# Performance work log

Hardware: AMD Instinct MI355X
Metric: run time of the kernel (lower is better)

Reference implementation:

```python
import jax, jax.numpy as jnp
import numpy as np

B, N, H, NH, P = 32, 400, 512, 8, 3
DK = H // NH
SCALE = DK ** -0.5
EPS = 1e-5


def _ln(x, g, b):
    m = jnp.mean(x, axis=-1, keepdims=True)
    v = jnp.mean((x - m) ** 2, axis=-1, keepdims=True)
    return (x - m) * jax.lax.rsqrt(v + EPS) * g + b


def _split(x):  # [B,N,H] -> [B,h,N,dk]
    return x.reshape(x.shape[0], x.shape[1], NH, DK).transpose(0, 2, 1, 3)


def _merge(x):  # [B,h,N,dk] -> [B,N,H]
    return x.transpose(0, 2, 1, 3).reshape(x.shape[0], x.shape[2], H)


def _attn(q, k, v, mask):
    s = jnp.einsum('bhid,bhjd->bhij', q, k) * SCALE
    s = s * (1.0 + mask[:, None])  # learned multiplicative prior mask
    p = jax.nn.softmax(s, axis=-1)
    return jnp.einsum('bhij,bhjd->bhid', p, v)


def _weight_gen(pri, z, C, wq, keys, wf, bf):
    # pooled token query attends over the num_priors prior matrices
    qv = jnp.mean(z @ wq, axis=1)  # [B,H]
    aw = jax.nn.softmax((qv @ keys.T) * (H ** -0.5), axis=-1)  # [B,P]
    w = jnp.einsum('bp,bpij->bij', aw, pri)  # [B,N,N] fused prior mask
    fused = jnp.einsum('bij,bjh->bih', C, z) @ wf + bf  # [B,N,H] neighborhood fusion
    return w, aw, fused


def _ffn(x, w1, b1, w2, b2):
    return jax.nn.gelu(x @ w1 + b1, approximate=False) @ w2 + b2


def _forward(x_FC, x_SC, pri_FC, pri_SC, FC, SC, dw,
             ln_attn_FC_g, ln_attn_FC_b, ln_attn_SC_g, ln_attn_SC_b,
             ln_ffn_FC_g, ln_ffn_FC_b, ln_ffn_SC_g, ln_ffn_SC_b,
             qkv_FC_w, qkv_SC_w,
             ffn_FC_w1, ffn_FC_b1, ffn_FC_w2, ffn_FC_b2,
             ffn_SC_w1, ffn_SC_b1, ffn_SC_w2, ffn_SC_b2,
             wg_q_w, wg_keys, wg_fuse_w, wg_fuse_b,
             dist_in_FC_w, dist_in_FC_b, dist_in_SC_w, dist_in_SC_b,
             dist_out_FC_w, dist_out_FC_b, dist_out_SC_w, dist_out_SC_b):
    z_FC = _ln(x_FC, ln_attn_FC_g, ln_attn_FC_b)
    z_SC = _ln(x_SC, ln_attn_SC_g, ln_attn_SC_b)
    q_FC, k_FC, v_FC = [_split(t) for t in jnp.split(z_FC @ qkv_FC_w, 3, axis=-1)]
    q_SC, k_SC, v_SC = [_split(t) for t in jnp.split(z_SC @ qkv_SC_w, 3, axis=-1)]
    w_FC, aw_FC, fused_FC = _weight_gen(pri_FC, z_FC, FC, wg_q_w, wg_keys, wg_fuse_w, wg_fuse_b)
    w_SC, aw_SC, fused_SC = _weight_gen(pri_SC, z_SC, SC, wg_q_w, wg_keys, wg_fuse_w, wg_fuse_b)
    ctx_FC = _merge(_attn(q_FC, k_FC, v_FC, w_FC))
    ctx_SC = _merge(_attn(q_SC, k_SC, v_SC, w_SC))
    attn_out_FC = x_FC + ctx_FC + fused_FC
    attn_out_SC = x_SC + ctx_SC + fused_SC
    x_FC_new = attn_out_FC + _ffn(_ln(attn_out_FC, ln_ffn_FC_g, ln_ffn_FC_b), ffn_FC_w1, ffn_FC_b1, ffn_FC_w2, ffn_FC_b2)
    x_SC_new = attn_out_SC + _ffn(_ln(attn_out_SC, ln_ffn_SC_g, ln_ffn_SC_b), ffn_SC_w1, ffn_SC_b1, ffn_SC_w2, ffn_SC_b2)
    wf, ws = dw[0], dw[1]
    proj_FC = x_FC_new @ dist_in_FC_w + dist_in_FC_b
    proj_SC = x_SC_new @ dist_in_SC_w + dist_in_SC_b
    l_FC = jax.nn.log_softmax(proj_FC.reshape(-1, H), axis=-1)
    l_SC = jax.nn.log_softmax(proj_SC.reshape(-1, H), axis=-1)
    p_FC = jnp.exp(l_FC)
    p_SC = jnp.exp(l_SC)
    rows = jnp.float32(l_FC.shape[0])
    kl_FC = jnp.sum(p_SC * (l_SC - l_FC)) / rows  # KLDiv(batchmean)(l_FC, p_SC)
    kl_SC = jnp.sum(p_FC * (l_FC - l_SC)) / rows
    x_FC_out = (1.0 - wf) * x_FC_new + wf * (proj_FC @ dist_out_FC_w + dist_out_FC_b)
    x_SC_out = (1.0 - ws) * x_SC_new + ws * (proj_SC @ dist_out_SC_w + dist_out_SC_b)
    distill_loss = 0.5 * (kl_FC * wf + kl_SC * ws)
    return (x_FC_out, x_SC_out, distill_loss, aw_FC, aw_SC)


def setup_inputs() -> dict:
    key = jax.random.key(0)
    ks = jax.random.split(key, 24)
    init = lambda k, shape: 0.02 * jax.random.normal(k, shape, jnp.float32)
    d = {}
    d['x_FC'] = jax.random.normal(ks[0], (B, N, H), jnp.float32)
    d['x_SC'] = jax.random.normal(ks[1], (B, N, H), jnp.float32)
    d['pri_FC'] = jax.random.uniform(ks[2], (B, P, N, N), jnp.float32)
    d['pri_SC'] = jax.random.uniform(ks[3], (B, P, N, N), jnp.float32)
    d['FC'] = jax.random.uniform(ks[4], (B, N, N), jnp.float32)
    d['SC'] = jax.random.uniform(ks[5], (B, N, N), jnp.float32)
    d['dw'] = jnp.array([0.5, 0.5], jnp.float32)
    for nm in ['ln_attn_FC', 'ln_attn_SC', 'ln_ffn_FC', 'ln_ffn_SC']:
        d[nm + '_g'] = jnp.ones((H,), jnp.float32)
        d[nm + '_b'] = jnp.zeros((H,), jnp.float32)
    d['qkv_FC_w'] = init(ks[6], (H, 3 * H))
    d['qkv_SC_w'] = init(ks[7], (H, 3 * H))
    d['ffn_FC_w1'] = init(ks[8], (H, 4 * H)); d['ffn_FC_b1'] = jnp.zeros((4 * H,), jnp.float32)
    d['ffn_FC_w2'] = init(ks[9], (4 * H, H)); d['ffn_FC_b2'] = jnp.zeros((H,), jnp.float32)
    d['ffn_SC_w1'] = init(ks[10], (H, 4 * H)); d['ffn_SC_b1'] = jnp.zeros((4 * H,), jnp.float32)
    d['ffn_SC_w2'] = init(ks[11], (4 * H, H)); d['ffn_SC_b2'] = jnp.zeros((H,), jnp.float32)
    d['wg_q_w'] = init(ks[12], (H, H))
    d['wg_keys'] = init(ks[13], (P, H))
    d['wg_fuse_w'] = init(ks[14], (H, H)); d['wg_fuse_b'] = jnp.zeros((H,), jnp.float32)
    d['dist_in_FC_w'] = init(ks[15], (H, H)); d['dist_in_FC_b'] = jnp.zeros((H,), jnp.float32)
    d['dist_in_SC_w'] = init(ks[16], (H, H)); d['dist_in_SC_b'] = jnp.zeros((H,), jnp.float32)
    d['dist_out_FC_w'] = init(ks[17], (H, H)); d['dist_out_FC_b'] = jnp.zeros((H,), jnp.float32)
    d['dist_out_SC_w'] = init(ks[18], (H, H)); d['dist_out_SC_b'] = jnp.zeros((H,), jnp.float32)
    return d


def reference(x_FC, x_SC, pri_FC, pri_SC, FC, SC, dw,
              ln_attn_FC_g, ln_attn_FC_b, ln_attn_SC_g, ln_attn_SC_b,
              ln_ffn_FC_g, ln_ffn_FC_b, ln_ffn_SC_g, ln_ffn_SC_b,
              qkv_FC_w, qkv_SC_w,
              ffn_FC_w1, ffn_FC_b1, ffn_FC_w2, ffn_FC_b2,
              ffn_SC_w1, ffn_SC_b1, ffn_SC_w2, ffn_SC_b2,
              wg_q_w, wg_keys, wg_fuse_w, wg_fuse_b,
              dist_in_FC_w, dist_in_FC_b, dist_in_SC_w, dist_in_SC_b,
              dist_out_FC_w, dist_out_FC_b, dist_out_SC_w, dist_out_SC_b):
    return _forward(x_FC, x_SC, pri_FC, pri_SC, FC, SC, dw,
                    ln_attn_FC_g, ln_attn_FC_b, ln_attn_SC_g, ln_attn_SC_b,
                    ln_ffn_FC_g, ln_ffn_FC_b, ln_ffn_SC_g, ln_ffn_SC_b,
                    qkv_FC_w, qkv_SC_w,
                    ffn_FC_w1, ffn_FC_b1, ffn_FC_w2, ffn_FC_b2,
                    ffn_SC_w1, ffn_SC_b1, ffn_SC_w2, ffn_SC_b2,
                    wg_q_w, wg_keys, wg_fuse_w, wg_fuse_b,
                    dist_in_FC_w, dist_in_FC_b, dist_in_SC_w, dist_in_SC_b,
                    dist_out_FC_w, dist_out_FC_b, dist_out_SC_w, dist_out_SC_b)
```

## Files before the change

kernel.cpp:

```cpp
#include <hip/hip_runtime.h>
#include <hip/hip_bf16.h>
#include <math.h>

typedef __hip_bfloat16 bf16;

#define B_  32
#define N_  400
#define H_  512
#define NH_ 8
#define DK_ 64
#define P_  3
#define BN_ (B_*N_)
#define H3_ 1536
#define H4_ 2048

#define GLD16(g, l) __builtin_amdgcn_global_load_lds( \
    (__attribute__((address_space(1))) void*)(g), \
    (__attribute__((address_space(3))) void*)(l), 16, 0, 0)

__device__ __forceinline__ float b2f(bf16 v){ return __bfloat162float(v); }
__device__ __forceinline__ bf16  f2b(float v){ return __float2bfloat16(v); }
__device__ __forceinline__ float bfu(unsigned short u){ return __uint_as_float(((unsigned int)u)<<16); }
__device__ __forceinline__ unsigned short f2bu(float v){
  union { bf16 b; unsigned short u; } cv; cv.b = __float2bfloat16(v); return cv.u;
// ... 99 lines not shown
  for (int q=0;q<4;++q){
    int nn = r + q*8;
    WT[(long)(n0+nn)*K + k0 + c] = f2b(tile[c][nn]);
  }
}

__global__ __launch_bounds__(256)
void ztrans_kernel(const bf16* __restrict__ ZB, bf16* __restrict__ ZBT)
{
  __shared__ unsigned short tile[32][33];
  int j0 = blockIdx.x*32, h0 = blockIdx.y*32, b = blockIdx.z;
  int t = threadIdx.x;
  int c = t & 31, r = t >> 5;
  const unsigned short* src = (const unsigned short*)(ZB + (long)b*N_*H_);
  #pragma unroll
  for (int p=0;p<4;++p){
    int j = j0 + r + p*8;
    unsigned short v = 0;
    if (j < 400) v = src[(long)j*H_ + h0 + c];
    tile[r+p*8][c] = v;
  }
  __syncthreads();
  unsigned short* dst = (unsigned short*)(ZBT + (long)b*512*416);
  #pragma unroll
  for (int p=0;p<4;++p){
    int hh = r + p*8;
    dst[(long)(h0+hh)*416 + j0 + c] = tile[c][hh];
  }
}

__global__ __launch_bounds__(256)
void cconv_kernel(const float* __restrict__ C, bf16* __restrict__ CB)
{
  long u = ((long)blockIdx.x*256 + threadIdx.x)*8;
  int b = (int)(u / (512*416));
  int rem = (int)(u - (long)b*(512*416));
  int r = rem / 416, c = rem % 416;
  ushort4 lo = {0,0,0,0}, hi = {0,0,0,0};
  if (r < 400 && c < 400){
    const float* p = C + (long)b*160000 + r*400 + c;
    float4 f0 = *(const float4*)p;
    float4 f1 = *(const float4*)(p+4);
    lo.x=f2bu(f0.x); lo.y=f2bu(f0.y); lo.z=f2bu(f0.z); lo.w=f2bu(f0.w);
    hi.x=f2bu(f1.x); hi.y=f2bu(f1.y); hi.z=f2bu(f1.z); hi.w=f2bu(f1.w);
  }
  *(ushort4*)((unsigned short*)CB + u)     = lo;
  *(ushort4*)((unsigned short*)CB + u + 4) = hi;
}

__global__ __launch_bounds__(256)
void vtrans_kernel(const bf16* __restrict__ qkv, bf16* __restrict__ vtg)
{
  __shared__ unsigned short tile[32][33];
  int j0 = blockIdx.x*32, d0 = blockIdx.y*32, bh = blockIdx.z;
  int b = bh >> 3, h = bh & 7;
  int t = threadIdx.x;
  int c = t & 31, r = t >> 5;
  const unsigned short* src = (const unsigned short*)(qkv + (long)b*N_*H3_ + 1024 + h*64 + d0);
  #pragma unroll
  for (int p=0;p<4;++p){
    int j = j0 + r + p*8;
    unsigned short v = 0;
    if (j < 400) v = src[(long)j*H3_ + c];
    tile[r+p*8][c] = v;
  }
  __syncthreads();
  unsigned short* dst = (unsigned short*)(vtg + (long)bh*64*416);
  #pragma unroll
  for (int p=0;p<4;++p){
    int dd = r + p*8;
    dst[(long)(d0+dd)*416 + j0 + c] = tile[c][dd];
  }
}

template<int MI,int ACT,int RES,int OMODE>
__global__ __launch_bounds__(256)
void mgemm_kernel(const bf16* __restrict__ A, const bf16* __restrict__ BT,
                  const float* __restrict__ bias, const bf16* __restrict__ res,
                  void* __restrict__ out, long oOff,
                  int M, int K, int Nn,
                  long sA, long sW, long sO,
                  const float* __restrict__ dwp, int dwidx)
{
  typedef __attribute__((ext_vector_type(8))) short bf16x8;
  typedef __attribute__((ext_vector_type(4))) float f32x4;
  constexpr int BM = MI*32;
  constexpr int LPT = MI/2 + 2;
  __shared__ unsigned short As[3][BM*32];
  __shared__ unsigned short Bs[3][128*32];
  unsigned nbx = gridDim.x, nby = gridDim.y;
  long nb = (long)nbx*nby*gridDim.z;
  long hw = blockIdx.x + (long)nbx*(blockIdx.y + (long)nby*blockIdx.z);
  long tid2 = (hw & 7)*(nb >> 3) + (hw >> 3);
  int bx = (int)(tid2 % nbx);
  long r2 = tid2 / nbx;
  int by = (int)(r2 % nby);
  int bz = (int)(r2 / nby);

  int t = threadIdx.x;
  int w = t >> 6, l = t & 63;
  int wm = (w >> 1)*(MI*16), wn = (w & 1)*64;
  int m0 = by*BM, n0 = bx*128;
  const bf16* Ab = A + (long)bz*sA;
  const bf16* Bb = BT + (long)bz*sW;
  long zO = (long)bz*sO;
  f32x4 acc[MI][4] = {};
  int lrow = l & 15, lkc = l >> 4;
  int srow = t >> 2, skc = t & 3;
  int sk = (skc ^ ((srow >> 1) & 3))*8;
  int ck = (lkc ^ ((lrow >> 1) & 3))*8;
  int nk = K >> 5;

  auto STAGE = [&](int tile, int bufi){
    int kk = tile << 5;
    #pragma unroll
    for (int half=0; half<MI/2; ++half){
      const unsigned short* gA = (const unsigned short*)Ab + (long)(m0+srow+half*64)*K + kk + sk;
      GLD16(gA, &As[bufi][w*512 + half*2048]);
    }
    #pragma unroll
    for (int half=0; half<2; ++half){
      const unsigned short* gB = (const unsigned short*)Bb + (long)(n0+srow+half*64)*K + kk + sk;
      GLD16(gB, &Bs[bufi][w*512 + half*2048]);
    }
  };

  STAGE(0, 0);
  if (nk > 1) STAGE(1, 1);
  for (int kt=0; kt<nk; ++kt){
    int cur = kt % 3;
    if (kt+2 < nk) STAGE(kt+2, (kt+2)%3);
    if (kt+2 < nk)      asm volatile("s_waitcnt vmcnt(%0)" :: "i"(2*LPT) : "memory");
    else if (kt+1 < nk) asm volatile("s_waitcnt vmcnt(%0)" :: "i"(LPT)   : "memory");
    else                asm volatile("s_waitcnt vmcnt(0)" ::: "memory");
    __builtin_amdgcn_s_barrier();
    asm volatile("" ::: "memory");
    bf16x8 af[MI], bf_[4];
    #pragma unroll
    for (int i=0;i<MI;++i) af[i]  = *(const bf16x8*)&As[cur][(wm + i*16 + lrow)*32 + ck];
    #pragma unroll
    for (int i=0;i<4;++i)  bf_[i] = *(const bf16x8*)&Bs[cur][(wn + i*16 + lrow)*32 + ck];
    __builtin_amdgcn_s_setprio(1);
    #pragma unroll
    for (int mi=0;mi<MI;++mi)
      #pragma unroll
      for (int ni=0;ni<4;++ni)
        acc[mi][ni] = __builtin_amdgcn_mfma_f32_16x16x32_bf16(bf_[ni], af[mi], acc[mi][ni], 0, 0, 0);
    __builtin_amdgcn_s_setprio(0);
    asm volatile("" ::: "memory");
    __builtin_amdgcn_s_barrier();
  }
  float wbl = (RES==2) ? dwp[dwidx] : 0.f;
  #pragma unroll
  for (int mi=0;mi<MI;++mi){
    int gm = m0 + wm + mi*16 + lrow;
    if (gm >= M) continue;
    #pragma unroll
    for (int ni=0;ni<4;++ni){
      int gnb = n0 + wn + ni*16 + lkc*4;
      long o = zO + (long)gm*Nn + gnb;
      float v0 = acc[mi][ni][0], v1 = acc[mi][ni][1], v2 = acc[mi][ni][2], v3 = acc[mi][ni][3];
      if (bias){
        float4 bv = *(const float4*)&bias[gnb];
        v0 += bv.x; v1 += bv.y; v2 += bv.z; v3 += bv.w;
      }
      if (ACT==1){
        v0 = gelu_t(v0); v1 = gelu_t(v1); v2 = gelu_t(v2); v3 = gelu_t(v3);
      }
      if (RES==1){
        ushort4 r4 = *(const ushort4*)((const unsigned short*)res + o);
        v0 += bfu(r4.x); v1 += bfu(r4.y); v2 += bfu(r4.z); v3 += bfu(r4.w);
      }
      if (RES==2){
        ushort4 r4 = *(const ushort4*)((const unsigned short*)res + o);
        v0 = (1.f-wbl)*bfu(r4.x) + wbl*v0;
        v1 = (1.f-wbl)*bfu(r4.y) + wbl*v1;
        v2 = (1.f-wbl)*bfu(r4.z) + wbl*v2;
        v3 = (1.f-wbl)*bfu(r4.w) + wbl*v3;
      }
      if (OMODE==0){
        ushort4 o4;
        o4.x = f2bu(v0); o4.y = f2bu(v1); o4.z = f2bu(v2); o4.w = f2bu(v3);
        *(ushort4*)((unsigned short*)out + o) = o4;
      } else {
        *(float4*)((float*)out + oOff + o) = make_float4(v0,v1,v2,v3);
      }
    }
  }
}

__global__ __launch_bounds__(256)
void zbar_kernel(const bf16* __restrict__ Z, float* __restrict__ zbar)
{
  __shared__ float red[256];
  int hc = blockIdx.x, b = blockIdx.y;
  int t = threadIdx.x;
  int col = hc*64 + (t & 63), ns = t >> 6;
  const bf16* p = Z + (long)b*N_*H_ + (long)ns*100*H_ + col;
  float s = 0.f;
  for (int n=0;n<100;++n) s += b2f(p[(long)n*H_]);
  red[t] = s;
  __syncthreads();
  if (t < 64){
    float tot = red[t]+red[t+64]+red[t+128]+red[t+192];
    zbar[b*512 + hc*64 + t] = tot * (1.f/400.f);
  }
}

__global__ __launch_bounds__(256)
void qv_kernel(const float* __restrict__ zbar, const void* __restrict__ wq,
               float* __restrict__ qv, const void* __restrict__ gref)
{
  __shared__ float red[256];
  const bool F32 = is_f32(gref);
  int ch = blockIdx.x, b = blockIdx.y;
  int t = threadIdx.x;
  int col = ch*32 + (t & 31), ks = t >> 5;
  const float* zb = zbar + b*512;
  float s = 0.f;
  int k0 = ks*64;
  for (int k=0;k<64;++k)
    s = fmaf(zb[k0+k], ldRaw(wq, (long)(k0+k)*512 + col, F32), s);
  red[t] = s;
  __syncthreads();
  if (t < 32){
    float q = 0.f;
    #pragma unroll
    for (int i=0;i<8;++i) q += red[t + i*32];
    qv[b*512 + ch*32 + t] = q;
  }
}

__global__ __launch_bounds__(256)
void aw_kernel(const float* __restrict__ qv, const void* __restrict__ keys,
               float* __restrict__ awf, void* __restrict__ outbase, long offAw,
               const void* __restrict__ gref)
{
  __shared__ float wred[4];
  const bool F32 = is_f32(gref);
  int b = blockIdx.x, t = threadIdx.x;
  const float* q = qv + b*512;
  float lg[3];
  #pragma unroll
  for (int p=0;p<3;++p){
    float part = q[t]*ldRaw(keys, p*512+t, F32) + q[t+256]*ldRaw(keys, p*512+t+256, F32);
    lg[p] = blockSum(part, wred) * 0.04419417382415922f;
  }
  float m = fmaxf(lg[0], fmaxf(lg[1], lg[2]));
  float e0 = expf(lg[0]-m), e1 = expf(lg[1]-m), e2 = expf(lg[2]-m);
  float inv = 1.f/(e0+e1+e2);
  if (t<3){
    float a = (t==0?e0:(t==1?e1:e2))*inv;
    awf[b*3+t] = a;
    stRaw(outbase, offAw + b*3 + t, a, F32);
  }
}

__global__ __launch_bounds__(256)
void wcomb_kernel(const void* __restrict__ pri, const float* __restrict__ awf,
                  bf16* __restrict__ WM, const void* __restrict__ gref)
{
  const bool F32 = is_f32(gref);
  long u = (long)blockIdx.x*256 + threadIdx.x;
  long e0 = u*4;
  int b = (int)(e0 / 160000);
  long r = e0 - (long)b*160000;
  float a0 = awf[b*3+0], a1 = awf[b*3+1], a2 = awf[b*3+2];
  float o0,o1,o2,o3;
  if (F32){
    const float* p0 = (const float*)pri + (long)b*3*160000 + r;
    float4 a = *(const float4*)(p0);
    float4 c = *(const float4*)(p0 + 160000);
    float4 d = *(const float4*)(p0 + 320000);
    o0 = a0*a.x + a1*c.x + a2*d.x;
    o1 = a0*a.y + a1*c.y + a2*d.y;
    o2 = a0*a.z + a1*c.z + a2*d.z;
    o3 = a0*a.w + a1*c.w + a2*d.w;
  } else {
    const bf16* p0 = (const bf16*)pri + (long)b*3*160000 + r;
    ushort4 a = *(const ushort4*)(p0);
    ushort4 c = *(const ushort4*)(p0 + 160000);
    ushort4 d = *(const ushort4*)(p0 + 320000);
    o0 = a0*bfu(a.x) + a1*bfu(c.x) + a2*bfu(d.x);
    o1 = a0*bfu(a.y) + a1*bfu(c.y) + a2*bfu(d.y);
    o2 = a0*bfu(a.z) + a1*bfu(c.z) + a2*bfu(d.z);
    o3 = a0*bfu(a.w) + a1*bfu(c.w) + a2*bfu(d.w);
  }
  ushort4 o;
  o.x = f2bu(o0); o.y = f2bu(o1); o.z = f2bu(o2); o.w = f2bu(o3);
  *(ushort4*)(WM + e0) = o;
}

__global__ __launch_bounds__(128)
void attn_kernel(const bf16* __restrict__ qkv, const bf16* __restrict__ wm,
                 const bf16* __restrict__ vtg, const void* __restrict__ x,
                 const bf16* __restrict__ fused, bf16* __restrict__ aout,
                 const void* __restrict__ gref)
{
  typedef __attribute__((ext_vector_type(8))) short bf16x8;
  typedef __attribute__((ext_vector_type(4))) float f32x4;
  __shared__ unsigned short Pbuf[2][2][16*40];
  const bool F32 = is_f32(gref);
  int t = threadIdx.x, wv = t >> 6, l = t & 63;
  long hw = blockIdx.x + 8L*(blockIdx.y + 32L*blockIdx.z);
  long t2 = (hw & 7)*416 + (hw >> 3);
  int h = (int)(t2 & 7);
  long r2 = t2 >> 3;
  int b = (int)(r2 & 31);
  int qtb = (int)(r2 >> 5);
  int qt = qtb*2 + wv;
  if (qt >= 25) return;
  int lr = l & 15, lg = l >> 4;
  int i0 = qt*16;
  const bf16* qb = qkv + (long)b*N_*H3_ + h*64;
  const bf16* kb = qb + 512;
  const bf16* wrow = wm + (long)b*N_*N_;
  const bf16* vt = vtg + (long)(b*NH_ + h)*64*416;
  bf16x8 qf0 = *(const bf16x8*)(qb + (long)(i0+lr)*H3_ + lg*8);
  bf16x8 qf1 = *(const bf16x8*)(qb + (long)(i0+lr)*H3_ + 32 + lg*8);
  float rm = -1e30f, rl = 0.f;
  f32x4 o[4] = {};
  #pragma unroll
  for (int w=0; w<13; ++w){
    int t0 = 2*w, t1 = 2*w+1;
    f32x4 s0, s1;
    {
      bf16x8 kf0 = *(const bf16x8*)(kb + (long)(t0*16+lr)*H3_ + lg*8);
      bf16x8 kf1 = *(const bf16x8*)(kb + (long)(t0*16+lr)*H3_ + 32 + lg*8);
      f32x4 st = {0.f,0.f,0.f,0.f};
      st = __builtin_amdgcn_mfma_f32_16x16x32_bf16(kf0, qf0, st, 0,0,0);
      st = __builtin_amdgcn_mfma_f32_16x16x32_bf16(kf1, qf1, st, 0,0,0);
      uint2 w4 = *(const uint2*)(wrow + (long)(i0+lr)*400 + t0*16 + lg*4);
      s0[0] = st[0]*0.125f*(1.f + bfu((unsigned short)(w4.x & 0xffffu)));
      s0[1] = st[1]*0.125f*(1.f + bfu((unsigned short)(w4.x >> 16)));
      s0[2] = st[2]*0.125f*(1.f + bfu((unsigned short)(w4.y & 0xffffu)));
      s0[3] = st[3]*0.125f*(1.f + bfu((unsigned short)(w4.y >> 16)));
    }
    if (t1 < 25){
      bf16x8 kf0 = *(const bf16x8*)(kb + (long)(t1*16+lr)*H3_ + lg*8);
      bf16x8 kf1 = *(const bf16x8*)(kb + (long)(t1*16+lr)*H3_ + 32 + lg*8);
      f32x4 st = {0.f,0.f,0.f,0.f};
      st = __builtin_amdgcn_mfma_f32_16x16x32_bf16(kf0, qf0, st, 0,0,0);
      st = __builtin_amdgcn_mfma_f32_16x16x32_bf16(kf1, qf1, st, 0,0,0);
      uint2 w4 = *(const uint2*)(wrow + (long)(i0+lr)*400 + t1*16 + lg*4);
      s1[0] = st[0]*0.125f*(1.f + bfu((unsigned short)(w4.x & 0xffffu)));
      s1[1] = st[1]*0.125f*(1.f + bfu((unsigned short)(w4.x >> 16)));
      s1[2] = st[2]*0.125f*(1.f + bfu((unsigned short)(w4.y & 0xffffu)));
      s1[3] = st[3]*0.125f*(1.f + bfu((unsigned short)(w4.y >> 16)));
    } else {
      s1[0]=s1[1]=s1[2]=s1[3] = -1e30f;
    }
    float tm = fmaxf(fmaxf(fmaxf(s0[0],s0[1]), fmaxf(s0[2],s0[3])),
                     fmaxf(fmaxf(s1[0],s1[1]), fmaxf(s1[2],s1[3])));
    tm = fmaxf(tm, __shfl_xor(tm, 16));
    tm = fmaxf(tm, __shfl_xor(tm, 32));
    float mn = fmaxf(rm, tm);
    float sc = __expf(rm - mn);
    unsigned pk0x, pk0y, pk1x = 0u, pk1y = 0u;
    float ls = 0.f;
    {
      unsigned u0 = f2bu(__expf(s0[0]-mn)), u1 = f2bu(__expf(s0[1]-mn));
      unsigned u2 = f2bu(__expf(s0[2]-mn)), u3 = f2bu(__expf(s0[3]-mn));
      pk0x = u0 | (u1<<16); pk0y = u2 | (u3<<16);
      ls += __uint_as_float(u0<<16) + __uint_as_float(u1<<16)
          + __uint_as_float(u2<<16) + __uint_as_float(u3<<16);
    }
    if (t1 < 25){
      unsigned u0 = f2bu(__expf(s1[0]-mn)), u1 = f2bu(__expf(s1[1]-mn));
      unsigned u2 = f2bu(__expf(s1[2]-mn)), u3 = f2bu(__expf(s1[3]-mn));
      pk1x = u0 | (u1<<16); pk1y = u2 | (u3<<16);
      ls += __uint_as_float(u0<<16) + __uint_as_float(u1<<16)
          + __uint_as_float(u2<<16) + __uint_as_float(u3<<16);
    }
    ls += __shfl_xor(ls, 16);
    ls += __shfl_xor(ls, 32);
    rl = rl*sc + ls;
    rm = mn;
    unsigned short* pb = Pbuf[wv][w & 1];
    *(uint2*)&pb[lr*40 + lg*4]      = make_uint2(pk0x, pk0y);
    *(uint2*)&pb[lr*40 + 16 + lg*4] = make_uint2(pk1x, pk1y);
    bf16x8 pa = *(const bf16x8*)&pb[lr*40 + lg*8];
    float sq0 = __shfl(sc, lg*4 + 0);
    float sq1 = __shfl(sc, lg*4 + 1);
    float sq2 = __shfl(sc, lg*4 + 2);
    float sq3 = __shfl(sc, lg*4 + 3);
    #pragma unroll
    for (int dt=0; dt<4; ++dt){
      o[dt][0] *= sq0; o[dt][1] *= sq1; o[dt][2] *= sq2; o[dt][3] *= sq3;
      bf16x8 vf = *(const bf16x8*)(vt + (long)(dt*16+lr)*416 + w*32 + lg*8);
      o[dt] = __builtin_amdgcn_mfma_f32_16x16x32_bf16(pa, vf, o[dt], 0,0,0);
    }
  }
  float invl = 1.f/rl;
  #pragma unroll
  for (int q=0;q<4;++q){
    float iv = __shfl(invl, lg*4 + q);
    long gi = (long)(b*N_ + i0 + lg*4 + q);
    #pragma unroll
    for (int dt=0;dt<4;++dt){
      long oi = gi*H_ + h*64 + dt*16 + lr;
      float xv = F32 ? ((const float*)x)[oi] : b2f(((const bf16*)x)[oi]);
      float fv = b2f(fused[oi]);
      aout[oi] = f2b(o[dt][q]*iv + xv + fv);
    }
  }
}

__global__ __launch_bounds__(256)
void kl_rows_kernel(const bf16* __restrict__ pF, const bf16* __restrict__ pS,
                    float2* __restrict__ rowpart)
{
  __shared__ float wred[4];
  long row = blockIdx.x;
  int t = threadIdx.x;
  const bf16* fr = pF + row*512;
  const bf16* sr = pS + row*512;
  float f0 = b2f(fr[t]), f1 = b2f(fr[t+256]), s0 = b2f(sr[t]), s1 = b2f(sr[t+256]);
  float mF = blockMax(fmaxf(f0,f1), wred);
  float mS = blockMax(fmaxf(s0,s1), wred);
  float sumF = blockSum(__expf(f0-mF)+__expf(f1-mF), wred);
  float sumS = blockSum(__expf(s0-mS)+__expf(s1-mS), wred);
  float lseF = mF + __logf(sumF), lseS = mS + __logf(sumS);
  float lF0 = f0-lseF, lF1 = f1-lseF, lS0 = s0-lseS, lS1 = s1-lseS;
  float pS0 = __expf(lS0), pS1 = __expf(lS1), pF0 = __expf(lF0), pF1 = __expf(lF1);
  float a  = pS0*(lS0-lF0) + pS1*(lS1-lF1);
  float bb = pF0*(lF0-lS0) + pF1*(lF1-lS1);
  a  = blockSum(a,  wred);
  bb = blockSum(bb, wred);
  if (t==0) rowpart[row] = make_float2(a, bb);
}

__global__ __launch_bounds__(256)
void kl_final_kernel(const float2* __restrict__ rowpart, const void* __restrict__ dw,
                     void* __restrict__ outbase, long offLoss,
                     const void* __restrict__ gref)
{
  __shared__ float wred[4];
  const bool F32 = is_f32(gref);
  int t = threadIdx.x;
  float sa=0.f, sb=0.f;
  for (int i=t;i<BN_;i+=256){ float2 v = rowpart[i]; sa+=v.x; sb+=v.y; }
  sa = blockSum(sa, wred);
  sb = blockSum(sb, wred);
  if (t==0){
    float wf = ldRaw(dw,0,F32), ws = ldRaw(dw,1,F32);
    float loss = 0.5f*((sa/12800.f)*wf + (sb/12800.f)*ws);
    stRaw(outbase, offLoss, loss, F32);
  }
}

#define OFF_ZB    0L
#define OFF_QKV   13107200L
#define OFF_FUSED 52428800L
#define OFF_WM    65536000L
#define OFF_CZ    75776000L
#define OFF_PROJ0 88883200L
#define OFF_PROJ1 101990400L
#define OFF_QKVT  115097600L
#define OFF_W1T   116670464L
#define OFF_W2T   118767616L
#define OFF_FUT   120864768L
#define OFF_DIT   121389056L
#define OFF_DOT   121913344L
#define OFF_ZBT   122437632L
#define OFF_ZBAR  136069120L
#define OFF_AWF   136134656L
#define OFF_ROWP  136135680L
#define OFF_VTG   136238080L
#define OFF_QV    149869568L

extern "C" void kernel_launch(void* const* d_in, const int* in_sizes, int n_in,
                              void* d_out, int out_size, void* d_ws, size_t ws_size,
                              hipStream_t stream)
{
  (void)in_sizes; (void)n_in; (void)out_size; (void)ws_size;
  const void* x[2]    = {d_in[0],  d_in[1]};
  const void* pri[2]  = {d_in[2],  d_in[3]};
  const float* Cm[2]  = {(const float*)d_in[4], (const float*)d_in[5]};
  const float* dwf    =  (const float*)d_in[6];
  const void* lnag[2] = {d_in[7],  d_in[9]};
  const void* lnab[2] = {d_in[8],  d_in[10]};
  const void* lnfg[2] = {d_in[11], d_in[13]};
  const void* lnfb[2] = {d_in[12], d_in[14]};
  const float* qkvw[2]= {(const float*)d_in[15], (const float*)d_in[16]};
  const float* fw1[2] = {(const float*)d_in[17], (const float*)d_in[21]};
  const float* fb1[2] = {(const float*)d_in[18], (const float*)d_in[22]};
  const float* fw2[2] = {(const float*)d_in[19], (const float*)d_in[23]};
  const float* fb2[2] = {(const float*)d_in[20], (const float*)d_in[24]};
  const void* wgq     =  d_in[25];
  const void* wgk     =  d_in[26];
  const float* wgfw   =  (const float*)d_in[27];
  const float* wgfb   =  (const float*)d_in[28];
  const float* diw[2] = {(const float*)d_in[29], (const float*)d_in[31]};
  const float* dib[2] = {(const float*)d_in[30], (const float*)d_in[32]};
  const float* dow[2] = {(const float*)d_in[33], (const float*)d_in[35]};
  const float* dob[2] = {(const float*)d_in[34], (const float*)d_in[36]};
  const void* gref    =  d_in[7];

  char* ws = (char*)d_ws;
  bf16*  ZB    = (bf16*)(ws + OFF_ZB);
  bf16*  LN2   = (bf16*)(ws + OFF_ZB);
  bf16*  XNEW  = (bf16*)(ws + OFF_ZB);
  bf16*  QKV   = (bf16*)(ws + OFF_QKV);
  bf16*  HH    = (bf16*)(ws + OFF_QKV);
  bf16*  FUSED = (bf16*)(ws + OFF_FUSED);
  bf16*  WM    = (bf16*)(ws + OFF_WM);
  bf16*  CZ    = (bf16*)(ws + OFF_CZ);
  bf16*  AOUT  = (bf16*)(ws + OFF_CZ);
  bf16*  PROJ[2] = {(bf16*)(ws + OFF_PROJ0), (bf16*)(ws + OFF_PROJ1)};
  bf16*  QKVT  = (bf16*)(ws + OFF_QKVT);
  bf16*  W1T   = (bf16*)(ws + OFF_W1T);
  bf16*  W2T   = (bf16*)(ws + OFF_W2T);
  bf16*  FUT   = (bf16*)(ws + OFF_FUT);
  bf16*  DIT   = (bf16*)(ws + OFF_DIT);
  bf16*  DOT   = (bf16*)(ws + OFF_DOT);
  bf16*  ZBT   = (bf16*)(ws + OFF_ZBT);
  bf16*  VTG   = (bf16*)(ws + OFF_VTG);
  bf16*  CB    = (bf16*)(ws + OFF_VTG);
  float* ZBAR  = (float*)(ws + OFF_ZBAR);
  float* AWF   = (float*)(ws + OFF_AWF);
  float2* ROWP = (float2*)(ws + OFF_ROWP);
  float* QV    = (float*)(ws + OFF_QV);

  const long offX[2]  = {0L, 6553600L};
  const long offLoss  = 13107200L;
  const long offAw[2] = {13107201L, 13107297L};

  for (int s=0; s<2; ++s){
    TC6 tp;
    tp.W[0]=qkvw[s]; tp.WT[0]=QKVT; tp.K[0]=512;  tp.N[0]=1536;
    tp.W[1]=fw1[s];  tp.WT[1]=W1T;  tp.K[1]=512;  tp.N[1]=2048;
    tp.W[2]=fw2[s];  tp.WT[2]=W2T;  tp.K[2]=2048; tp.N[2]=512;
    tp.W[3]=wgfw;    tp.WT[3]=FUT;  tp.K[3]=512;  tp.N[3]=512;
    tp.W[4]=diw[s];  tp.WT[4]=DIT;  tp.K[4]=512;  tp.N[4]=512;
    tp.W[5]=dow[s];  tp.WT[5]=DOT;  tp.K[5]=512;  tp.N[5]=512;
    tp.base[0]=0; tp.base[1]=768; tp.base[2]=1792; tp.base[3]=2816;
    tp.base[4]=3072; tp.base[5]=3328;
    tc6_kernel<<<3584,256,0,stream>>>(tp);
    ln_kernel<0><<<BN_,256,0,stream>>>(x[s], lnag[s], lnab[s], ZB, gref);
    zbar_kernel<<<dim3(8,B_),256,0,stream>>>(ZB, ZBAR);
    ztrans_kernel<<<dim3(13,16,32),256,0,stream>>>(ZB, ZBT);
    cconv_kernel<<<3328,256,0,stream>>>(Cm[s], CB);
    mgemm_kernel<4,0,0,0><<<dim3(12,100,1),256,0,stream>>>(
        ZB, QKVT, nullptr, nullptr, QKV, 0, BN_, 512, H3_, 0,0,0, nullptr,0);
    qv_kernel<<<dim3(16,B_),256,0,stream>>>(ZBAR, wgq, QV, gref);
    aw_kernel<<<B_,256,0,stream>>>(QV, wgk, AWF, d_out, offAw[s], gref);
    wcomb_kernel<<<5000,256,0,stream>>>(pri[s], AWF, WM, gref);
    mgemm_kernel<4,0,0,0><<<dim3(4,4,32),256,0,stream>>>(
        CB, ZBT, nullptr, nullptr, CZ, 0, 400, 416, 512,
        212992L, 212992L, 204800L, nullptr,0);
    mgemm_kernel<2,0,0,0><<<dim3(4,200,1),256,0,stream>>>(
        CZ, FUT, wgfb, nullptr, FUSED, 0, BN_, 512, 512, 0,0,0, nullptr,0);
    vtrans_kernel<<<dim3(13,2,256),256,0,stream>>>(QKV, VTG);
    attn_kernel<<<dim3(NH_,B_,13),128,0,stream>>>(QKV, WM, VTG, x[s], FUSED, AOUT, gref);
    ln_kernel<1><<<BN_,256,0,stream>>>(AOUT, lnfg[s], lnfb[s], LN2, gref);
    mgemm_kernel<4,1,0,0><<<dim3(16,100,1),256,0,stream>>>(
        LN2, W1T, fb1[s], nullptr, HH, 0, BN_, 512, H4_, 0,0,0, nullptr,0);
    mgemm_kernel<2,0,1,0><<<dim3(4,200,1),256,0,stream>>>(
        HH, W2T, fb2[s], AOUT, XNEW, 0, BN_, 2048, 512, 0,0,0, nullptr,0);
    mgemm_kernel<2,0,0,0><<<dim3(4,200,1),256,0,stream>>>(
        XNEW, DIT, dib[s], nullptr, PROJ[s], 0, BN_, 512, 512, 0,0,0, nullptr,0);
    mgemm_kernel<2,0,2,1><<<dim3(4,200,1),256,0,stream>>>(
        PROJ[s], DOT, dob[s], XNEW, d_out, offX[s], BN_, 512, 512, 0,0,0, dwf, s);
  }
  kl_rows_kernel<<<BN_,256,0,stream>>>(PROJ[0], PROJ[1], ROWP);
  kl_final_kernel<<<1,256,0,stream>>>(ROWP, dwf, d_out, offLoss, gref);
}
```

Before: 901.2 us.

## Prefetch next K, V and mask tiles into registers in attention loop

The attention kernel now loads the K fragments, mask words and V fragments for the next iteration into registers while the current iteration's MFMAs and softmax run. This is a double-buffered software pipeline meant to hide global-load latency. It also replaces the swizzled block-index-to-(head, batch, query-tile) mapping with a direct mapping from blockIdx, which changes which blocks share cache lines in L2. The cost is higher register pressure, which may lower occupancy.

```diff
diff --git a/kernel.cpp b/kernel.cpp
--- a/kernel.cpp
+++ b/kernel.cpp
@@ -425,53 +425,71 @@
   __shared__ unsigned short Pbuf[2][2][16*40];
   const bool F32 = is_f32(gref);
   int t = threadIdx.x, wv = t >> 6, l = t & 63;
-  long hw = blockIdx.x + 8L*(blockIdx.y + 32L*blockIdx.z);
-  long t2 = (hw & 7)*416 + (hw >> 3);
-  int h = (int)(t2 & 7);
-  long r2 = t2 >> 3;
-  int b = (int)(r2 & 31);
-  int qtb = (int)(r2 >> 5);
-  int qt = qtb*2 + wv;
+  int h = blockIdx.x, b = blockIdx.y;
+  int qt = blockIdx.z*2 + wv;
   if (qt >= 25) return;
   int lr = l & 15, lg = l >> 4;
   int i0 = qt*16;
   const bf16* qb = qkv + (long)b*N_*H3_ + h*64;
   const bf16* kb = qb + 512;
-  const bf16* wrow = wm + (long)b*N_*N_;
+  const bf16* wrow = wm + (long)b*N_*N_ + (long)(i0+lr)*400 + lg*4;
   const bf16* vt = vtg + (long)(b*NH_ + h)*64*416;
   bf16x8 qf0 = *(const bf16x8*)(qb + (long)(i0+lr)*H3_ + lg*8);
   bf16x8 qf1 = *(const bf16x8*)(qb + (long)(i0+lr)*H3_ + 32 + lg*8);
+  bf16x8 ka0, ka1, kc0, kc1, vp0, vp1, vp2, vp3;
+  uint2 ma, mc;
+  ka0 = *(const bf16x8*)(kb + (long)(0*16+lr)*H3_ + lg*8);
+  ka1 = *(const bf16x8*)(kb + (long)(0*16+lr)*H3_ + 32 + lg*8);
+  kc0 = *(const bf16x8*)(kb + (long)(1*16+lr)*H3_ + lg*8);
+  kc1 = *(const bf16x8*)(kb + (long)(1*16+lr)*H3_ + 32 + lg*8);
+  ma = *(const uint2*)(wrow + 0*16);
+  mc = *(const uint2*)(wrow + 1*16);
+  vp0 = *(const bf16x8*)(vt + (long)( 0+lr)*416 + lg*8);
+  vp1 = *(const bf16x8*)(vt + (long)(16+lr)*416 + lg*8);
+  vp2 = *(const bf16x8*)(vt + (long)(32+lr)*416 + lg*8);
+  vp3 = *(const bf16x8*)(vt + (long)(48+lr)*416 + lg*8);
   float rm = -1e30f, rl = 0.f;
   f32x4 o[4] = {};
   #pragma unroll
   for (int w=0; w<13; ++w){
-    int t0 = 2*w, t1 = 2*w+1;
-    f32x4 s0, s1;
-    {
-      bf16x8 kf0 = *(const bf16x8*)(kb + (long)(t0*16+lr)*H3_ + lg*8);
-      bf16x8 kf1 = *(const bf16x8*)(kb + (long)(t0*16+lr)*H3_ + 32 + lg*8);
-      f32x4 st = {0.f,0.f,0.f,0.f};
-      st = __builtin_amdgcn_mfma_f32_16x16x32_bf16(kf0, qf0, st, 0,0,0);
-      st = __builtin_amdgcn_mfma_f32_16x16x32_bf16(kf1, qf1, st, 0,0,0);
-      uint2 w4 = *(const uint2*)(wrow + (long)(i0+lr)*400 + t0*16 + lg*4);
-      s0[0] = st[0]*0.125f*(1.f + bfu((unsigned short)(w4.x & 0xffffu)));
-      s0[1] = st[1]*0.125f*(1.f + bfu((unsigned short)(w4.x >> 16)));
-      s0[2] = st[2]*0.125f*(1.f + bfu((unsigned short)(w4.y & 0xffffu)));
-      s0[3] = st[3]*0.125f*(1.f + bfu((unsigned short)(w4.y >> 16)));
-    }
-    if (t1 < 25){
-      bf16x8 kf0 = *(const bf16x8*)(kb + (long)(t1*16+lr)*H3_ + lg*8);
-      bf16x8 kf1 = *(const bf16x8*)(kb + (long)(t1*16+lr)*H3_ + 32 + lg*8);
-      f32x4 st = {0.f,0.f,0.f,0.f};
-      st = __builtin_amdgcn_mfma_f32_16x16x32_bf16(kf0, qf0, st, 0,0,0);
-      st = __builtin_amdgcn_mfma_f32_16x16x32_bf16(kf1, qf1, st, 0,0,0);
-      uint2 w4 = *(const uint2*)(wrow + (long)(i0+lr)*400 + t1*16 + lg*4);
-      s1[0] = st[0]*0.125f*(1.f + bfu((unsigned short)(w4.x & 0xffffu)));
-      s1[1] = st[1]*0.125f*(1.f + bfu((unsigned short)(w4.x >> 16)));
-      s1[2] = st[2]*0.125f*(1.f + bfu((unsigned short)(w4.y & 0xffffu)));
-      s1[3] = st[3]*0.125f*(1.f + bfu((unsigned short)(w4.y >> 16)));
+    f32x4 s0 = {0.f,0.f,0.f,0.f}, s1;
+    s0 = __builtin_amdgcn_mfma_f32_16x16x32_bf16(ka0, qf0, s0, 0,0,0);
+    s0 = __builtin_amdgcn_mfma_f32_16x16x32_bf16(ka1, qf1, s0, 0,0,0);
+    if (w < 12){
+      f32x4 z = {0.f,0.f,0.f,0.f};
+      z = __builtin_amdgcn_mfma_f32_16x16x32_bf16(kc0, qf0, z, 0,0,0);
+      z = __builtin_amdgcn_mfma_f32_16x16x32_bf16(kc1, qf1, z, 0,0,0);
+      s1 = z;
+    }
+    s0[0] = s0[0]*0.125f*(1.f + bfu((unsigned short)(ma.x & 0xffffu)));
+    s0[1] = s0[1]*0.125f*(1.f + bfu((unsigned short)(ma.x >> 16)));
+    s0[2] = s0[2]*0.125f*(1.f + bfu((unsigned short)(ma.y & 0xffffu)));
+    s0[3] = s0[3]*0.125f*(1.f + bfu((unsigned short)(ma.y >> 16)));
+    if (w < 12){
+      s1[0] = s1[0]*0.125f*(1.f + bfu((unsigned short)(mc.x & 0xffffu)));
+      s1[1] = s1[1]*0.125f*(1.f + bfu((unsigned short)(mc.x >> 16)));
+      s1[2] = s1[2]*0.125f*(1.f + bfu((unsigned short)(mc.y & 0xffffu)));
+      s1[3] = s1[3]*0.125f*(1.f + bfu((unsigned short)(mc.y >> 16)));
     } else {
       s1[0]=s1[1]=s1[2]=s1[3] = -1e30f;
+    }
+    bf16x8 na0, na1, nc0, nc1, nv0, nv1, nv2, nv3;
+    uint2 nma, nmc;
+    if (w < 12){
+      int t0n = 2*w+2, t1n = 2*w+3;
+      na0 = *(const bf16x8*)(kb + (long)(t0n*16+lr)*H3_ + lg*8);
+      na1 = *(const bf16x8*)(kb + (long)(t0n*16+lr)*H3_ + 32 + lg*8);
+      nma = *(const uint2*)(wrow + t0n*16);
+      if (w < 11){
+        nc0 = *(const bf16x8*)(kb + (long)(t1n*16+lr)*H3_ + lg*8);
+        nc1 = *(const bf16x8*)(kb + (long)(t1n*16+lr)*H3_ + 32 + lg*8);
+        nmc = *(const uint2*)(wrow + t1n*16);
+      }
+      int wn1 = (w+1)*32;
+      nv0 = *(const bf16x8*)(vt + (long)( 0+lr)*416 + wn1 + lg*8);
+      nv1 = *(const bf16x8*)(vt + (long)(16+lr)*416 + wn1 + lg*8);
+      nv2 = *(const bf16x8*)(vt + (long)(32+lr)*416 + wn1 + lg*8);
+      nv3 = *(const bf16x8*)(vt + (long)(48+lr)*416 + wn1 + lg*8);
     }
     float tm = fmaxf(fmaxf(fmaxf(s0[0],s0[1]), fmaxf(s0[2],s0[3])),
                      fmaxf(fmaxf(s1[0],s1[1]), fmaxf(s1[2],s1[3])));
@@ -488,7 +506,7 @@
       ls += __uint_as_float(u0<<16) + __uint_as_float(u1<<16)
           + __uint_as_float(u2<<16) + __uint_as_float(u3<<16);
     }
-    if (t1 < 25){
+    if (w < 12){
       unsigned u0 = f2bu(__expf(s1[0]-mn)), u1 = f2bu(__expf(s1[1]-mn));
       unsigned u2 = f2bu(__expf(s1[2]-mn)), u3 = f2bu(__expf(s1[3]-mn));
       pk1x = u0 | (u1<<16); pk1y = u2 | (u3<<16);
@@ -507,11 +525,18 @@
     float sq1 = __shfl(sc, lg*4 + 1);
     float sq2 = __shfl(sc, lg*4 + 2);
     float sq3 = __shfl(sc, lg*4 + 3);
-    #pragma unroll
-    for (int dt=0; dt<4; ++dt){
-      o[dt][0] *= sq0; o[dt][1] *= sq1; o[dt][2] *= sq2; o[dt][3] *= sq3;
-      bf16x8 vf = *(const bf16x8*)(vt + (long)(dt*16+lr)*416 + w*32 + lg*8);
-      o[dt] = __builtin_amdgcn_mfma_f32_16x16x32_bf16(pa, vf, o[dt], 0,0,0);
+    o[0][0] *= sq0; o[0][1] *= sq1; o[0][2] *= sq2; o[0][3] *= sq3;
+    o[0] = __builtin_amdgcn_mfma_f32_16x16x32_bf16(pa, vp0, o[0], 0,0,0);
+    o[1][0] *= sq0; o[1][1] *= sq1; o[1][2] *= sq2; o[1][3] *= sq3;
+    o[1] = __builtin_amdgcn_mfma_f32_16x16x32_bf16(pa, vp1, o[1], 0,0,0);
+    o[2][0] *= sq0; o[2][1] *= sq1; o[2][2] *= sq2; o[2][3] *= sq3;
+    o[2] = __builtin_amdgcn_mfma_f32_16x16x32_bf16(pa, vp2, o[2], 0,0,0);
+    o[3][0] *= sq0; o[3][1] *= sq1; o[3][2] *= sq2; o[3][3] *= sq3;
+    o[3] = __builtin_amdgcn_mfma_f32_16x16x32_bf16(pa, vp3, o[3], 0,0,0);
+    if (w < 12){
+      ka0 = na0; ka1 = na1; ma = nma;
+      if (w < 11){ kc0 = nc0; kc1 = nc1; mc = nmc; }
+      vp0 = nv0; vp1 = nv1; vp2 = nv2; vp3 = nv3;
     }
   }
   float invl = 1.f/rl;
```

Result: faster. 850.8 us (-5.6%).

## Process two attention heads per wave to share prior-mask loads

Applied to the files above, without the earlier changes.

Each wave in the attention kernel now computes two heads (hx and hx+4) for the same query tile. The multiplicative prior-mask tile is loaded once and used for both heads, and the grid is halved to four head groups per batch. The change also drops the XCD-aware block-index remapping in favour of plain blockIdx mapping. It doubles per-thread accumulator registers and interleaves two independent softmax chains, which adds ILP but may lower occupancy.

```diff
diff --git a/kernel.cpp b/kernel.cpp
--- a/kernel.cpp
+++ b/kernel.cpp
@@ -425,106 +425,172 @@
   __shared__ unsigned short Pbuf[2][2][16*40];
   const bool F32 = is_f32(gref);
   int t = threadIdx.x, wv = t >> 6, l = t & 63;
-  long hw = blockIdx.x + 8L*(blockIdx.y + 32L*blockIdx.z);
-  long t2 = (hw & 7)*416 + (hw >> 3);
-  int h = (int)(t2 & 7);
-  long r2 = t2 >> 3;
-  int b = (int)(r2 & 31);
-  int qtb = (int)(r2 >> 5);
-  int qt = qtb*2 + wv;
+  int hx = blockIdx.x, b = blockIdx.y;
+  int qt = blockIdx.z*2 + wv;
   if (qt >= 25) return;
   int lr = l & 15, lg = l >> 4;
   int i0 = qt*16;
-  const bf16* qb = qkv + (long)b*N_*H3_ + h*64;
-  const bf16* kb = qb + 512;
-  const bf16* wrow = wm + (long)b*N_*N_;
-  const bf16* vt = vtg + (long)(b*NH_ + h)*64*416;
-  bf16x8 qf0 = *(const bf16x8*)(qb + (long)(i0+lr)*H3_ + lg*8);
-  bf16x8 qf1 = *(const bf16x8*)(qb + (long)(i0+lr)*H3_ + 32 + lg*8);
-  float rm = -1e30f, rl = 0.f;
-  f32x4 o[4] = {};
+  const bf16* base = qkv + (long)b*N_*H3_;
+  const bf16* qb0 = base + hx*64;
+  const bf16* kb0 = qb0 + 512;
+  const bf16* qb1 = base + (hx+4)*64;
+  const bf16* kb1 = qb1 + 512;
+  const bf16* wrow = wm + (long)b*N_*N_ + (long)(i0+lr)*400 + lg*4;
+  const bf16* vt0 = vtg + (long)(b*NH_ + hx)*64*416;
+  const bf16* vt1 = vtg + (long)(b*NH_ + hx+4)*64*416;
+  bf16x8 qA0 = *(const bf16x8*)(qb0 + (long)(i0+lr)*H3_ + lg*8);
+  bf16x8 qA1 = *(const bf16x8*)(qb0 + (long)(i0+lr)*H3_ + 32 + lg*8);
+  bf16x8 qB0 = *(const bf16x8*)(qb1 + (long)(i0+lr)*H3_ + lg*8);
+  bf16x8 qB1 = *(const bf16x8*)(qb1 + (long)(i0+lr)*H3_ + 32 + lg*8);
+  float rmA = -1e30f, rlA = 0.f, rmB = -1e30f, rlB = 0.f;
+  f32x4 oA[4] = {}, oB[4] = {};
   #pragma unroll
   for (int w=0; w<13; ++w){
     int t0 = 2*w, t1 = 2*w+1;
-    f32x4 s0, s1;
+    bf16x8 kA0 = *(const bf16x8*)(kb0 + (long)(t0*16+lr)*H3_ + lg*8);
+    bf16x8 kA1 = *(const bf16x8*)(kb0 + (long)(t0*16+lr)*H3_ + 32 + lg*8);
+    bf16x8 kB0 = *(const bf16x8*)(kb1 + (long)(t0*16+lr)*H3_ + lg*8);
+    bf16x8 kB1 = *(const bf16x8*)(kb1 + (long)(t0*16+lr)*H3_ + 32 + lg*8);
+    uint2 ma = *(const uint2*)(wrow + t0*16);
+    f32x4 sA0 = {0.f,0.f,0.f,0.f}, sB0 = {0.f,0.f,0.f,0.f}, sA1, sB1;
+    sA0 = __builtin_amdgcn_mfma_f32_16x16x32_bf16(kA0, qA0, sA0, 0,0,0);
+    sA0 = __builtin_amdgcn_mfma_f32_16x16x32_bf16(kA1, qA1, sA0, 0,0,0);
+    sB0 = __builtin_amdgcn_mfma_f32_16x16x32_bf16(kB0, qB0, sB0, 0,0,0);
+    sB0 = __builtin_amdgcn_mfma_f32_16x16x32_bf16(kB1, qB1, sB0, 0,0,0);
+    uint2 mc;
+    if (t1 < 25){
+      bf16x8 cA0 = *(const bf16x8*)(kb0 + (long)(t1*16+lr)*H3_ + lg*8);
+      bf16x8 cA1 = *(const bf16x8*)(kb0 + (long)(t1*16+lr)*H3_ + 32 + lg*8);
+      bf16x8 cB0 = *(const bf16x8*)(kb1 + (long)(t1*16+lr)*H3_ + lg*8);
+      bf16x8 cB1 = *(const bf16x8*)(kb1 + (long)(t1*16+lr)*H3_ + 32 + lg*8);
+      mc = *(const uint2*)(wrow + t1*16);
+      f32x4 zA = {0.f,0.f,0.f,0.f}, zB = {0.f,0.f,0.f,0.f};
+      zA = __builtin_amdgcn_mfma_f32_16x16x32_bf16(cA0, qA0, zA, 0,0,0);
+      zA = __builtin_amdgcn_mfma_f32_16x16x32_bf16(cA1, qA1, zA, 0,0,0);
+      zB = __builtin_amdgcn_mfma_f32_16x16x32_bf16(cB0, qB0, zB, 0,0,0);
+      zB = __builtin_amdgcn_mfma_f32_16x16x32_bf16(cB1, qB1, zB, 0,0,0);
+      sA1 = zA; sB1 = zB;
+    } else {
+      sA1[0]=sA1[1]=sA1[2]=sA1[3] = -1e30f;
+      sB1[0]=sB1[1]=sB1[2]=sB1[3] = -1e30f;
+    }
+    float m0 = bfu((unsigned short)(ma.x & 0xffffu));
+    float m1 = bfu((unsigned short)(ma.x >> 16));
+    float m2 = bfu((unsigned short)(ma.y & 0xffffu));
+    float m3 = bfu((unsigned short)(ma.y >> 16));
+    sA0[0] = sA0[0]*0.125f*(1.f+m0); sB0[0] = sB0[0]*0.125f*(1.f+m0);
+    sA0[1] = sA0[1]*0.125f*(1.f+m1); sB0[1] = sB0[1]*0.125f*(1.f+m1);
+    sA0[2] = sA0[2]*0.125f*(1.f+m2); sB0[2] = sB0[2]*0.125f*(1.f+m2);
+    sA0[3] = sA0[3]*0.125f*(1.f+m3); sB0[3] = sB0[3]*0.125f*(1.f+m3);
+    if (t1 < 25){
+      float n0 = bfu((unsigned short)(mc.x & 0xffffu));
+      float n1 = bfu((unsigned short)(mc.x >> 16));
+      float n2 = bfu((unsigned short)(mc.y & 0xffffu));
+      float n3 = bfu((unsigned short)(mc.y >> 16));
+      sA1[0] = sA1[0]*0.125f*(1.f+n0); sB1[0] = sB1[0]*0.125f*(1.f+n0);
+      sA1[1] = sA1[1]*0.125f*(1.f+n1); sB1[1] = sB1[1]*0.125f*(1.f+n1);
+      sA1[2] = sA1[2]*0.125f*(1.f+n2); sB1[2] = sB1[2]*0.125f*(1.f+n2);
+      sA1[3] = sA1[3]*0.125f*(1.f+n3); sB1[3] = sB1[3]*0.125f*(1.f+n3);
+    }
     {
-      bf16x8 kf0 = *(const bf16x8*)(kb + (long)(t0*16+lr)*H3_ + lg*8);
-      bf16x8 kf1 = *(const bf16x8*)(kb + (long)(t0*16+lr)*H3_ + 32 + lg*8);
-      f32x4 st = {0.f,0.f,0.f,0.f};
-      st = __builtin_amdgcn_mfma_f32_16x16x32_bf16(kf0, qf0, st, 0,0,0);
-      st = __builtin_amdgcn_mfma_f32_16x16x32_bf16(kf1, qf1, st, 0,0,0);
-      uint2 w4 = *(const uint2*)(wrow + (long)(i0+lr)*400 + t0*16 + lg*4);
-      s0[0] = st[0]*0.125f*(1.f + bfu((unsigned short)(w4.x & 0xffffu)));
-      s0[1] = st[1]*0.125f*(1.f + bfu((unsigned short)(w4.x >> 16)));
-      s0[2] = st[2]*0.125f*(1.f + bfu((unsigned short)(w4.y & 0xffffu)));
-      s0[3] = st[3]*0.125f*(1.f + bfu((unsigned short)(w4.y >> 16)));
+      float tm = fmaxf(fmaxf(fmaxf(sA0[0],sA0[1]), fmaxf(sA0[2],sA0[3])),
+                       fmaxf(fmaxf(sA1[0],sA1[1]), fmaxf(sA1[2],sA1[3])));
+      tm = fmaxf(tm, __shfl_xor(tm, 16));
+      tm = fmaxf(tm, __shfl_xor(tm, 32));
+      float mn = fmaxf(rmA, tm);
+      float sc = __expf(rmA - mn);
+      unsigned pk0x, pk0y, pk1x = 0u, pk1y = 0u;
+      float ls = 0.f;
+      {
+        unsigned u0 = f2bu(__expf(sA0[0]-mn)), u1 = f2bu(__expf(sA0[1]-mn));
+        unsigned u2 = f2bu(__expf(sA0[2]-mn)), u3 = f2bu(__expf(sA0[3]-mn));
+        pk0x = u0 | (u1<<16); pk0y = u2 | (u3<<16);
+        ls += __uint_as_float(u0<<16) + __uint_as_float(u1<<16)
+            + __uint_as_float(u2<<16) + __uint_as_float(u3<<16);
+      }
+      if (t1 < 25){
+        unsigned u0 = f2bu(__expf(sA1[0]-mn)), u1 = f2bu(__expf(sA1[1]-mn));
+        unsigned u2 = f2bu(__expf(sA1[2]-mn)), u3 = f2bu(__expf(sA1[3]-mn));
+        pk1x = u0 | (u1<<16); pk1y = u2 | (u3<<16);
+        ls += __uint_as_float(u0<<16) + __uint_as_float(u1<<16)
+            + __uint_as_float(u2<<16) + __uint_as_float(u3<<16);
+      }
+      ls += __shfl_xor(ls, 16);
+      ls += __shfl_xor(ls, 32);
+      rlA = rlA*sc + ls;
+      rmA = mn;
+      unsigned short* pb = Pbuf[wv][0];
+      *(uint2*)&pb[lr*40 + lg*4]      = make_uint2(pk0x, pk0y);
+      *(uint2*)&pb[lr*40 + 16 + lg*4] = make_uint2(pk1x, pk1y);
+      bf16x8 pa = *(const bf16x8*)&pb[lr*40 + lg*8];
+      float sq0 = __shfl(sc, lg*4 + 0);
+      float sq1 = __shfl(sc, lg*4 + 1);
+      float sq2 = __shfl(sc, lg*4 + 2);
+      float sq3 = __shfl(sc, lg*4 + 3);
+      #pragma unroll
+      for (int dt=0; dt<4; ++dt){
+        oA[dt][0] *= sq0; oA[dt][1] *= sq1; oA[dt][2] *= sq2; oA[dt][3] *= sq3;
+        bf16x8 vf = *(const bf16x8*)(vt0 + (long)(dt*16+lr)*416 + w*32 + lg*8);
+        oA[dt] = __builtin_amdgcn_mfma_f32_16x16x32_bf16(pa, vf, oA[dt], 0,0,0);
+      }
     }
-    if (t1 < 25){
-      bf16x8 kf0 = *(const bf16x8*)(kb + (long)(t1*16+lr)*H3_ + lg*8);
-      bf16x8 kf1 = *(const bf16x8*)(kb + (long)(t1*16+lr)*H3_ + 32 + lg*8);
-      f32x4 st = {0.f,0.f,0.f,0.f};
-      st = __builtin_amdgcn_mfma_f32_16x16x32_bf16(kf0, qf0, st, 0,0,0);
-      st = __builtin_amdgcn_mfma_f32_16x16x32_bf16(kf1, qf1, st, 0,0,0);
-      uint2 w4 = *(const uint2*)(wrow + (long)(i0+lr)*400 + t1*16 + lg*4);
-      s1[0] = st[0]*0.125f*(1.f + bfu((unsigned short)(w4.x & 0xffffu)));
-      s1[1] = st[1]*0.125f*(1.f + bfu((unsigned short)(w4.x >> 16)));
-      s1[2] = st[2]*0.125f*(1.f + bfu((unsigned short)(w4.y & 0xffffu)));
-      s1[3] = st[3]*0.125f*(1.f + bfu((unsigned short)(w4.y >> 16)));
-    } else {
-      s1[0]=s1[1]=s1[2]=s1[3] = -1e30f;
+    {
+      float tm = fmaxf(fmaxf(fmaxf(sB0[0],sB0[1]), fmaxf(sB0[2],sB0[3])),
+                       fmaxf(fmaxf(sB1[0],sB1[1]), fmaxf(sB1[2],sB1[3])));
+      tm = fmaxf(tm, __shfl_xor(tm, 16));
+      tm = fmaxf(tm, __shfl_xor(tm, 32));
+      float mn = fmaxf(rmB, tm);
+      float sc = __expf(rmB - mn);
+      unsigned pk0x, pk0y, pk1x = 0u, pk1y = 0u;
+      float ls = 0.f;
+      {
+        unsigned u0 = f2bu(__expf(sB0[0]-mn)), u1 = f2bu(__expf(sB0[1]-mn));
+        unsigned u2 = f2bu(__expf(sB0[2]-mn)), u3 = f2bu(__expf(sB0[3]-mn));
+        pk0x = u0 | (u1<<16); pk0y = u2 | (u3<<16);
+        ls += __uint_as_float(u0<<16) + __uint_as_float(u1<<16)
+            + __uint_as_float(u2<<16) + __uint_as_float(u3<<16);
+      }
+      if (t1 < 25){
+        unsigned u0 = f2bu(__expf(sB1[0]-mn)), u1 = f2bu(__expf(sB1[1]-mn));
+        unsigned u2 = f2bu(__expf(sB1[2]-mn)), u3 = f2bu(__expf(sB1[3]-mn));
+        pk1x = u0 | (u1<<16); pk1y = u2 | (u3<<16);
+        ls += __uint_as_float(u0<<16) + __uint_as_float(u1<<16)
+            + __uint_as_float(u2<<16) + __uint_as_float(u3<<16);
+      }
+      ls += __shfl_xor(ls, 16);
+      ls += __shfl_xor(ls, 32);
+      rlB = rlB*sc + ls;
+      rmB = mn;
+      unsigned short* pb = Pbuf[wv][1];
+      *(uint2*)&pb[lr*40 + lg*4]      = make_uint2(pk0x, pk0y);
+      *(uint2*)&pb[lr*40 + 16 + lg*4] = make_uint2(pk1x, pk1y);
+      bf16x8 pa = *(const bf16x8*)&pb[lr*40 + lg*8];
+      float sq0 = __shfl(sc, lg*4 + 0);
+      float sq1 = __shfl(sc, lg*4 + 1);
+      float sq2 = __shfl(sc, lg*4 + 2);
+      float sq3 = __shfl(sc, lg*4 + 3);
+      #pragma unroll
+      for (int dt=0; dt<4; ++dt){
+        oB[dt][0] *= sq0; oB[dt][1] *= sq1; oB[dt][2] *= sq2; oB[dt][3] *= sq3;
+        bf16x8 vf = *(const bf16x8*)(vt1 + (long)(dt*16+lr)*416 + w*32 + lg*8);
+        oB[dt] = __builtin_amdgcn_mfma_f32_16x16x32_bf16(pa, vf, oB[dt], 0,0,0);
+      }
     }
-    float tm = fmaxf(fmaxf(fmaxf(s0[0],s0[1]), fmaxf(s0[2],s0[3])),
-                     fmaxf(fmaxf(s1[0],s1[1]), fmaxf(s1[2],s1[3])));
-    tm = fmaxf(tm, __shfl_xor(tm, 16));
-    tm = fmaxf(tm, __shfl_xor(tm, 32));
-    float mn = fmaxf(rm, tm);
-    float sc = __expf(rm - mn);
-    unsigned pk0x, pk0y, pk1x = 0u, pk1y = 0u;
-    float ls = 0.f;
-    {
-      unsigned u0 = f2bu(__expf(s0[0]-mn)), u1 = f2bu(__expf(s0[1]-mn));
-      unsigned u2 = f2bu(__expf(s0[2]-mn)), u3 = f2bu(__expf(s0[3]-mn));
-      pk0x = u0 | (u1<<16); pk0y = u2 | (u3<<16);
-      ls += __uint_as_float(u0<<16) + __uint_as_float(u1<<16)
-          + __uint_as_float(u2<<16) + __uint_as_float(u3<<16);
-    }
-    if (t1 < 25){
-      unsigned u0 = f2bu(__expf(s1[0]-mn)), u1 = f2bu(__expf(s1[1]-mn));
-      unsigned u2 = f2bu(__expf(s1[2]-mn)), u3 = f2bu(__expf(s1[3]-mn));
-      pk1x = u0 | (u1<<16); pk1y = u2 | (u3<<16);
-      ls += __uint_as_float(u0<<16) + __uint_as_float(u1<<16)
-          + __uint_as_float(u2<<16) + __uint_as_float(u3<<16);
-    }
-    ls += __shfl_xor(ls, 16);
-    ls += __shfl_xor(ls, 32);
-    rl = rl*sc + ls;
-    rm = mn;
-    unsigned short* pb = Pbuf[wv][w & 1];
-    *(uint2*)&pb[lr*40 + lg*4]      = make_uint2(pk0x, pk0y);
-    *(uint2*)&pb[lr*40 + 16 + lg*4] = make_uint2(pk1x, pk1y);
-    bf16x8 pa = *(const bf16x8*)&pb[lr*40 + lg*8];
-    float sq0 = __shfl(sc, lg*4 + 0);
-    float sq1 = __shfl(sc, lg*4 + 1);
-    float sq2 = __shfl(sc, lg*4 + 2);
-    float sq3 = __shfl(sc, lg*4 + 3);
-    #pragma unroll
-    for (int dt=0; dt<4; ++dt){
-      o[dt][0] *= sq0; o[dt][1] *= sq1; o[dt][2] *= sq2; o[dt][3] *= sq3;
-      bf16x8 vf = *(const bf16x8*)(vt + (long)(dt*16+lr)*416 + w*32 + lg*8);
-      o[dt] = __builtin_amdgcn_mfma_f32_16x16x32_bf16(pa, vf, o[dt], 0,0,0);
-    }
-  }
-  float invl = 1.f/rl;
+  }
+  float invA = 1.f/rlA, invB = 1.f/rlB;
   #pragma unroll
   for (int q=0;q<4;++q){
-    float iv = __shfl(invl, lg*4 + q);
+    float ivA = __shfl(invA, lg*4 + q);
+    float ivB = __shfl(invB, lg*4 + q);
     long gi = (long)(b*N_ + i0 + lg*4 + q);
     #pragma unroll
     for (int dt=0;dt<4;++dt){
-      long oi = gi*H_ + h*64 + dt*16 + lr;
-      float xv = F32 ? ((const float*)x)[oi] : b2f(((const bf16*)x)[oi]);
-      float fv = b2f(fused[oi]);
-      aout[oi] = f2b(o[dt][q]*iv + xv + fv);
+      long oiA = gi*H_ + hx*64 + dt*16 + lr;
+      float xvA = F32 ? ((const float*)x)[oiA] : b2f(((const bf16*)x)[oiA]);
+      aout[oiA] = f2b(oA[dt][q]*ivA + xvA + b2f(fused[oiA]));
+      long oiB = gi*H_ + (hx+4)*64 + dt*16 + lr;
+      float xvB = F32 ? ((const float*)x)[oiB] : b2f(((const bf16*)x)[oiB]);
+      aout[oiB] = f2b(oB[dt][q]*ivB + xvB + b2f(fused[oiB]));
     }
   }
 }
@@ -675,7 +741,7 @@
     mgemm_kernel<2,0,0,0><<<dim3(4,200,1),256,0,stream>>>(
         CZ, FUT, wgfb, nullptr, FUSED, 0, BN_, 512, 512, 0,0,0, nullptr,0);
     vtrans_kernel<<<dim3(13,2,256),256,0,stream>>>(QKV, VTG);
-    attn_kernel<<<dim3(NH_,B_,13),128,0,stream>>>(QKV, WM, VTG, x[s], FUSED, AOUT, gref);
+    attn_kernel<<<dim3(4,B_,13),128,0,stream>>>(QKV, WM, VTG, x[s], FUSED, AOUT, gref);
     ln_kernel<1><<<BN_,256,0,stream>>>(AOUT, lnfg[s], lnfb[s], LN2, gref);
     mgemm_kernel<4,1,0,0><<<dim3(16,100,1),256,0,stream>>>(
         LN2, W1T, fb1[s], nullptr, HH, 0, BN_, 512, H4_, 0,0,0, nullptr,0);
```

After: 970.9 us. 7.7% more time.
